# Optimization experiments

Hardware: AMD Instinct MI355X
Metric: run time of the kernel (lower is better)

Reference implementation:

```python
import jax, jax.numpy as jnp
import numpy as np

N_HEADS = 32
N_KV = 8
HEAD_DIM = 128
EPS = 1e-5

def _rope(t, fr, fi):
    # t: [b,s,h,hd] -> pairs [b,s,h,hd/2,2]; fr/fi: [s,hd/2]
    tp = t.astype(jnp.float32).reshape(*t.shape[:-1], HEAD_DIM // 2, 2)
    a, b = tp[..., 0], tp[..., 1]
    fr = fr[None, :, None, :]
    fi = fi[None, :, None, :]
    out = jnp.stack([a * fr - b * fi, a * fi + b * fr], axis=-1)
    return out.reshape(t.shape).astype(t.dtype)

def _rmsnorm(t):
    tf = t.astype(jnp.float32)
    return (tf * jax.lax.rsqrt(jnp.mean(tf * tf, axis=-1, keepdims=True) + EPS)).astype(t.dtype)

def setup_inputs() -> dict:
    key = jax.random.key(0)
    ks = jax.random.split(key, 5)
    b, s, dim = 1, 2048, 4096
    x = jax.random.normal(ks[0], (b, s, dim), dtype=jnp.float32) * 0.02
    wq = jax.random.normal(ks[1], (dim, dim), dtype=jnp.float32) * 0.02
    wk = jax.random.normal(ks[2], (N_KV * HEAD_DIM, dim), dtype=jnp.float32) * 0.02
    wv = jax.random.normal(ks[3], (N_KV * HEAD_DIM, dim), dtype=jnp.float32) * 0.02
    wo = jax.random.normal(ks[4], (dim, dim), dtype=jnp.float32) * 0.02
    # RoPE freqs, llama-style theta=10000
    inv = 1.0 / (10000.0 ** (np.arange(0, HEAD_DIM, 2, dtype=np.float32) / HEAD_DIM))
    ang = np.outer(np.arange(s, dtype=np.float32), inv)  # [s, hd/2]
    freqs_cis = jnp.asarray(np.stack([np.cos(ang), np.sin(ang)], axis=-1))  # [s, hd/2, 2]
    # causal additive mask
    mask = jnp.where(jnp.tril(jnp.ones((s, s), dtype=bool)), 0.0, -1e30).astype(jnp.float32)
    return {"x": x, "wq": wq, "wk": wk, "wv": wv, "wo": wo,
            "freqs_cis": freqs_cis, "mask": mask, "start_pos": 0}

def reference(x, wq, wk, wv, wo, freqs_cis, mask, start_pos):
    b, s, dim = x.shape
    n_rep = N_HEADS // N_KV
    xq = jnp.einsum('bsd,ed->bse', x, wq).reshape(b, s, N_HEADS, HEAD_DIM)
    xk = jnp.einsum('bsd,ed->bse', x, wk).reshape(b, s, N_KV, HEAD_DIM)
    xv = jnp.einsum('bsd,ed->bse', x, wv).reshape(b, s, N_KV, HEAD_DIM)
    fr, fi = freqs_cis[..., 0], freqs_cis[..., 1]
    xq = _rope(xq, fr, fi)
    xk = _rope(xk, fr, fi)
    xq = _rmsnorm(xq)
    xk = _rmsnorm(xk)
    # start_pos=0 prefill: KV cache write/read is identity on xk/xv
    q = xq.transpose(0, 2, 1, 3).reshape(b, N_KV, n_rep, s, HEAD_DIM)  # grouped query heads
    k = xk.transpose(0, 2, 1, 3)  # [b, n_kv, s, hd]
    v = xv.transpose(0, 2, 1, 3)
    scores = jnp.einsum('bkrsd,bktd->bkrst', q, k) / np.sqrt(HEAD_DIM)
    scores = scores + mask[None, None, None, :, :]
    probs = jax.nn.softmax(scores, axis=-1)
    o = jnp.einsum('bkrst,bktd->bkrsd', probs, v)
    o = o.reshape(b, N_HEADS, s, HEAD_DIM).transpose(0, 2, 1, 3).reshape(b, s, dim)
    return jnp.einsum('bse,de->bsd', o, wo)
```

## Files before the change

### kernel.cpp

```cpp
#include <hip/hip_runtime.h>
#include <hip/hip_bf16.h>
#include <cstdint>
#include <cstddef>

using u16 = unsigned short;
using u32 = unsigned int;
using u64 = unsigned long long;

typedef __attribute__((ext_vector_type(8))) __bf16 bf16x8;
typedef __attribute__((ext_vector_type(4))) float f32x4;
typedef __attribute__((ext_vector_type(2))) float f32x2;
typedef __attribute__((ext_vector_type(4))) u32 u32x4;

typedef const __attribute__((address_space(1))) void* gas_ptr;
typedef __attribute__((address_space(3))) void* las_ptr;

__device__ __forceinline__ void async_cp16(const void* g, void* l) {
  __builtin_amdgcn_global_load_lds((gas_ptr)g, (las_ptr)l, 16, 0, 0);
}

__device__ __forceinline__ float bf2f(u16 u) {
  u32 v = ((u32)u) << 16;
  return __builtin_bit_cast(float, v);
}
__device__ __forceinline__ u16 f2bf(float f) {
  u32 v = __builtin_bit_cast(u32, f);
  u32 r = (v + 0x7fffu + ((v >> 16) & 1u)) >> 16;
  return (u16)r;
}

__device__ __forceinline__ f32x4 mfma16(bf16x8 a, bf16x8 b, f32x4 c) {
  return __builtin_amdgcn_mfma_f32_16x16x32_bf16(a, b, c, 0, 0, 0);
}

__global__ __launch_bounds__(256) void cvt4(const float* __restrict__ x,
                                            const float* __restrict__ wq,
                                            const float* __restrict__ wk,
                                            const float* __restrict__ wv,
                                            u16* __restrict__ xb,
                                            u16* __restrict__ wqkv) {
  const int B0 = 1048576;
  const int B1 = B0 + 2097152;
  const int B2 = B1 + 524288;
  const int B3 = B2 + 524288;
  int i = blockIdx.x * blockDim.x + threadIdx.x;
  int stride = gridDim.x * blockDim.x;
  for (; i < B3; i += stride) {
    const float* src; u16* dst; int j;
    if (i < B0)      { src = x;  dst = xb;                           j = i; }
    else if (i < B1) { src = wq; dst = wqkv;                         j = i - B0; }
    else if (i < B2) { src = wk; dst = wqkv + (size_t)4096 * 4096;   j = i - B1; }
    else             { src = wv; dst = wqkv + (size_t)5120 * 4096;   j = i - B2; }
    const float4* p = (const float4*)(src + (size_t)j * 8);
    float4 a = p[0], b = p[1];
    union { u16 us[8]; u32x4 v; } o;
    o.us[0] = f2bf(a.x); o.us[1] = f2bf(a.y); o.us[2] = f2bf(a.z); o.us[3] = f2bf(a.w);
    o.us[4] = f2bf(b.x); o.us[5] = f2bf(b.y); o.us[6] = f2bf(b.z); o.us[7] = f2bf(b.w);
    *(u32x4*)(dst + (size_t)j * 8) = o.v;
  }
}

__global__ __launch_bounds__(512, 2) void gemm256(const u16* __restrict__ A,
                                                  const u16* __restrict__ B,
                                                  int M, int N, int K,
                                                  u16* __restrict__ qh,
                                                  u16* __restrict__ khh,
                                                  u16* __restrict__ vt,
                                                  const float* __restrict__ freqs) {
  __shared__ __align__(16) u16 As[2][16384];
  __shared__ __align__(16) u16 Bs[2][16384];
  const int tid = threadIdx.x;
  const int wave = tid >> 6, lane = tid & 63;
  const int quad = lane >> 4, c16 = lane & 15;
  const int wr = wave >> 2, wc = wave & 3;

  const int mb = M >> 8;
  const int nb = N >> 8;
  const int per_xcd_n = nb >> 3;
  const int xcd = blockIdx.x & 7, lid = blockIdx.x >> 3;
  const int m_t = lid % mb, n_local = lid / mb;
  const int m0 = m_t * 256, n0 = (xcd * per_xcd_n + n_local) * 256;

  const u16* Ab = A + (size_t)m0 * K;
  const u16* Bb = B + (size_t)n0 * K;

  f32x4 acc[8][4] = {};

  const int atg = wc * 64 + lane;
  const int bh = wc >> 1;
  const int btg = (((wr << 1) | (wc & 1)) << 6) + lane;

  auto stage_tile = [&](int k0, int b) __attribute__((always_inline)) {
#pragma unroll
    for (int j = 0; j < 4; ++j) {
      int idx = atg + 256 * j;
      int rl = idx >> 3;
      int row = wr * 128 + rl;
      int sg = (idx & 7) ^ (row & 7);
      async_cp16(Ab + (size_t)row * K + k0 + sg * 8, &As[b][wr * 8192 + idx * 8]);
    }
#pragma unroll
    for (int j = 0; j < 4; ++j) {
      int idx = btg + 256 * j;
      int rl = idx >> 3;
      int row = bh * 128 + rl;
      int sg = (idx & 7) ^ (row & 7);
      async_cp16(Bb + (size_t)row * K + k0 + sg * 8, &Bs[b][bh * 8192 + idx * 8]);
    }
  };

  bf16x8 bfr[4];
  auto phase = [&](int b, int ks, int mh, bool loadB) __attribute__((always_inline)) {
    bf16x8 af[4];
    if (loadB) {
#pragma unroll
      for (int nt = 0; nt < 4; ++nt) {
        int row = wc * 64 + nt * 16 + c16;
        bfr[nt] = *(const bf16x8*)(&Bs[b][row * 64 + (((ks * 4 + quad) ^ (row & 7)) * 8)]);
      }
    }
#pragma unroll
    for (int mt = 0; mt < 4; ++mt) {
      int row = wr * 128 + (mh * 4 + mt) * 16 + c16;
      af[mt] = *(const bf16x8*)(&As[b][row * 64 + (((ks * 4 + quad) ^ (row & 7)) * 8)]);
    }
    asm volatile("s_waitcnt lgkmcnt(0)" ::: "memory");
    __builtin_amdgcn_sched_barrier(0);
    __builtin_amdgcn_s_setprio(1);
#pragma unroll
    for (int mt = 0; mt < 4; ++mt)
#pragma unroll
      for (int nt = 0; nt < 4; ++nt)
        acc[mh * 4 + mt][nt] = mfma16(af[mt], bfr[nt], acc[mh * 4 + mt][nt]);
    __builtin_amdgcn_s_setprio(0);
    __builtin_amdgcn_s_barrier();
  };

  const int nk = K >> 6;
  stage_tile(0, 0);

#pragma unroll 1
  for (int t = 0; t < nk; ++t) {
    const int b = t & 1;
    const int k0 = t << 6;
    if (t + 1 < nk) {
      stage_tile(k0 + 64, b ^ 1);
      asm volatile("s_waitcnt vmcnt(8)" ::: "memory");
    } else {
      asm volatile("s_waitcnt vmcnt(0)" ::: "memory");
    }
    __builtin_amdgcn_s_barrier();
    phase(b, 0, 0, true);
    phase(b, 0, 1, false);
    phase(b, 1, 0, true);
    phase(b, 1, 1, false);
  }

  __syncthreads();
  float* sums = (float*)&As[0][0];
  if (n0 < 5120) {
    float ss_arr[8][4];
    const int dbase = (wc & 1) * 64;
#pragma unroll
    for (int mt = 0; mt < 8; ++mt) {
#pragma unroll
      for (int r = 0; r < 4; ++r) {
        int s = m0 + wr * 128 + mt * 16 + quad * 4 + r;
        const float* fb = freqs + (size_t)s * 128;
        float ssv = 0.0f;
#pragma unroll
        for (int nt = 0; nt < 4; ++nt) {
          int d = dbase + nt * 16 + c16;
          float v = acc[mt][nt][r];
          float p = __shfl_xor(v, 1, 64);
          f32x2 ff = *(const f32x2*)(fb + (d & ~1));
          float res = (c16 & 1) ? fmaf(v, ff.x, p * ff.y)
                                : fmaf(v, ff.x, -p * ff.y);
          acc[mt][nt][r] = res;
          ssv = fmaf(res, res, ssv);
        }
#pragma unroll
        for (int m = 1; m < 16; m <<= 1) ssv += __shfl_xor(ssv, m, 64);
        ss_arr[mt][r] = ssv;
      }
    }
    if (c16 == 0) {
#pragma unroll
      for (int mt = 0; mt < 8; ++mt)
#pragma unroll
        for (int r = 0; r < 4; ++r)
          sums[wc * 256 + wr * 128 + mt * 16 + quad * 4 + r] = ss_arr[mt][r];
    }
    __syncthreads();
    const int head_col = n0 + wc * 64;
    u16* outb = (head_col < 4096)
                    ? (qh + (size_t)(head_col >> 7) * M * 128)
                    : (khh + (size_t)((head_col - 4096) >> 7) * M * 128);
#pragma unroll
    for (int mt = 0; mt < 8; ++mt) {
#pragma unroll
      for (int r = 0; r < 4; ++r) {
        int rl = wr * 128 + mt * 16 + quad * 4 + r;
        float tot = ss_arr[mt][r] + sums[(wc ^ 1) * 256 + rl];
        float scl = rsqrtf(tot * (1.0f / 128.0f) + 1e-5f);
        int s = m0 + rl;
#pragma unroll
        for (int nt = 0; nt < 4; ++nt)
          outb[(size_t)s * 128 + dbase + nt * 16 + c16] = f2bf(acc[mt][nt][r] * scl);
      }
    }
  } else {
#pragma unroll
    for (int mt = 0; mt < 8; ++mt) {
#pragma unroll
      for (int nt = 0; nt < 4; ++nt) {
        int dv = (n0 - 5120) + wc * 64 + nt * 16 + c16;
        int s0 = m0 + wr * 128 + mt * 16 + quad * 4;
        union { u16 us[4]; u64 v; } pk;
#pragma unroll
        for (int r = 0; r < 4; ++r) pk.us[r] = f2bf(acc[mt][nt][r]);
        *(u64*)(vt + (size_t)dv * M + s0) = pk.v;
      }
    }
  }
}

__global__ __launch_bounds__(256, 3) void gemm_out(const u16* __restrict__ A,
                                                   const u16* __restrict__ B,
                                                   float* __restrict__ C,
                                                   int M, int N, int K) {
  __shared__ __align__(16) u16 As[128 * 64];
  __shared__ __align__(16) u16 Bs[128 * 64];
  const int tid = threadIdx.x;
  const int wave = tid >> 6, lane = tid & 63;
  const int quad = lane >> 4, c16 = lane & 15;

  const int mb = M >> 7, nb = N >> 7;
  const int per_xcd_n = nb >> 3;
  const int xcd = blockIdx.x & 7, lid = blockIdx.x >> 3;
  const int m_t = lid % mb, n_local = lid / mb;
  const int m0 = m_t * 128, n0 = (xcd * per_xcd_n + n_local) * 128;

  const int wm = (wave & 1) * 64, wn = (wave >> 1) * 64;

  f32x4 acc[4][4] = {};

  const u16* Ab = A + (size_t)m0 * K;
  const u16* Bb = B + (size_t)n0 * K;

  for (int k0 = 0; k0 < K; k0 += 64) {
    __syncthreads();
#pragma unroll
    for (int i = 0; i < 4; ++i) {
      int idx = tid + 256 * i;
      int row = idx >> 3, sg = (idx & 7) ^ (row & 7);
      async_cp16(Ab + (size_t)row * K + k0 + sg * 8, As + (size_t)idx * 8);
    }
#pragma unroll
    for (int i = 0; i < 4; ++i) {
      int idx = tid + 256 * i;
      int row = idx >> 3, sg = (idx & 7) ^ (row & 7);
      async_cp16(Bb + (size_t)row * K + k0 + sg * 8, Bs + (size_t)idx * 8);
    }
    asm volatile("s_waitcnt vmcnt(0)" ::: "memory");
    __syncthreads();

    bf16x8 af[4][2], bfr[4][2];
#pragma unroll
    for (int mt = 0; mt < 4; ++mt) {
      int row = wm + mt * 16 + c16;
#pragma unroll
      for (int c = 0; c < 2; ++c)
        af[mt][c] = *(const bf16x8*)(As + row * 64 + (((c * 4 + quad) ^ (row & 7)) * 8));
    }
#pragma unroll
    for (int nt = 0; nt < 4; ++nt) {
      int row = wn + nt * 16 + c16;
#pragma unroll
      for (int c = 0; c < 2; ++c)
        bfr[nt][c] = *(const bf16x8*)(Bs + row * 64 + (((c * 4 + quad) ^ (row & 7)) * 8));
    }
#pragma unroll
    for (int c = 0; c < 2; ++c)
#pragma unroll
      for (int mt = 0; mt < 4; ++mt)
#pragma unroll
        for (int nt = 0; nt < 4; ++nt)
          acc[mt][nt] = mfma16(af[mt][c], bfr[nt][c], acc[mt][nt]);
  }

#pragma unroll
  for (int mt = 0; mt < 4; ++mt) {
#pragma unroll
    for (int nt = 0; nt < 4; ++nt) {
#pragma unroll
      for (int r = 0; r < 4; ++r) {
        int gm = m0 + wm + mt * 16 + quad * 4 + r;
        int gn = n0 + wn + nt * 16 + c16;
        C[(size_t)gm * N + gn] = acc[mt][nt][r];
      }
    }
  }
}

#define SEQ 2048
__global__ __launch_bounds__(512, 2) void attn(const u16* __restrict__ Q,
                                               const u16* __restrict__ Kh,
                                               const u16* __restrict__ VT,
                                               u16* __restrict__ O,
                                               const float* __restrict__ wo,
                                               u16* __restrict__ wob) {
  __shared__ __align__(16) u16 Ks[2][64 * 128];
  __shared__ __align__(16) u16 Vs[2][128 * 64];
  __shared__ __align__(16) u16 Ps[8][32 * 64];
  const int tid = threadIdx.x;
  const int wave = tid >> 6, lane = tid & 63;
  const int quad = lane >> 4, c16 = lane & 15;
  const int bid = blockIdx.x;
  const int hk = bid & 7;
  const int rest = bid >> 3;
  const int hq = rest & 3;
  const int p = rest >> 2;
  const int h = hk * 4 + hq;

  const int wl = wave & 3, grp = wave >> 2;
  const int qt = grp ? p : (15 - p);
  const int q0w = qt * 128 + wl * 32;
  const int kend = (15 - p) * 128 + 128;

  const float sc = 0.12751743f;
  const float B = 16.5f;
  const u16* Kb = Kh + (size_t)hk * SEQ * 128;
  const u16* Vb = VT + (size_t)hk * 128 * SEQ;

  auto stage = [&](int t0, int b) __attribute__((always_inline)) {
#pragma unroll
    for (int i = 0; i < 2; ++i) {
      int idx = tid + 512 * i;
      int row = idx >> 4, sg = (idx & 15) ^ (row & 7);
      async_cp16(Kb + (size_t)(t0 + row) * 128 + sg * 8, &Ks[b][(size_t)idx * 8]);
    }
#pragma unroll
    for (int i = 0; i < 2; ++i) {
      int idx = tid + 512 * i;
      int row = idx >> 3, sg = (idx & 7) ^ (row & 7);
      async_cp16(Vb + (size_t)row * SEQ + t0 + sg * 8, &Vs[b][(size_t)idx * 8]);
    }
  };

  bf16x8 qfr[2][4];
  const u16* qbase = Q + (size_t)h * SEQ * 128;
#pragma unroll
  for (int g = 0; g < 2; ++g)
#pragma unroll
    for (int c = 0; c < 4; ++c)
      qfr[g][c] =
          *(const bf16x8*)(qbase + (size_t)(q0w + g * 16 + c16) * 128 + c * 32 + quad * 8);

  f32x4 o_acc[2][8] = {};
  float lsum[2][4] = {};

  stage(0, 0);

#pragma unroll 1
  for (int t0 = 0; t0 < kend; t0 += 64) {
    const int cur = (t0 >> 6) & 1;
    asm volatile("s_waitcnt vmcnt(0)" ::: "memory");
    __syncthreads();
    if (t0 + 64 < kend) stage(t0 + 64, cur ^ 1);

    if (t0 < q0w + 32) {
      f32x4 sa[2][4] = {};
      __builtin_amdgcn_s_setprio(1);
#pragma unroll
      for (int ct = 0; ct < 4; ++ct) {
        int t = ct * 16 + c16;
        int tbase = t * 128;
        int tsw = t & 7;
#pragma unroll
        for (int c = 0; c < 4; ++c) {
          bf16x8 kf = *(const bf16x8*)(&Ks[cur][tbase + (((c * 4 + quad) ^ tsw) * 8)]);
          sa[0][ct] = mfma16(qfr[0][c], kf, sa[0][ct]);
          sa[1][ct] = mfma16(qfr[1][c], kf, sa[1][ct]);
        }
      }
      __builtin_amdgcn_s_setprio(0);

      const bool diag = (t0 + 64 > q0w);
      auto soft = [&](bool masked) __attribute__((always_inline)) {
#pragma unroll
        for (int g = 0; g < 2; ++g) {
#pragma unroll
          for (int r = 0; r < 4; ++r) {
            int row = g * 16 + quad * 4 + r;
            int row_q = q0w + row;
            int rbase = row * 64;
            int rsw = row & 7;
#pragma unroll
            for (int ct = 0; ct < 4; ++ct) {
              float s = sa[g][ct][r];
              float arg = fmaf(s, sc, -B);
              if (masked) {
                int t_idx = t0 + ct * 16 + c16;
                arg = (t_idx <= row_q) ? arg : -1.0e30f;
              }
              float pe = exp2f(arg);
              lsum[g][r] += pe;
              u32 pb = (__builtin_bit_cast(u32, pe) + 0x8000u) >> 16;
              Ps[wave][rbase + (((ct * 2 + (c16 >> 3)) ^ rsw) * 8) + (c16 & 7)] = (u16)pb;
            }
          }
        }
      };
      if (diag) soft(true); else soft(false);
      asm volatile("s_waitcnt lgkmcnt(0)" ::: "memory");

      __builtin_amdgcn_s_setprio(1);
#pragma unroll
      for (int tc = 0; tc < 2; ++tc) {
        bf16x8 pf[2];
#pragma unroll
        for (int g = 0; g < 2; ++g) {
          int prow = g * 16 + c16;
          pf[g] = *(const bf16x8*)(&Ps[wave][prow * 64 + (((tc * 4 + quad) ^ (prow & 7)) * 8)]);
        }
#pragma unroll
        for (int nt = 0; nt < 8; ++nt) {
          int dl = nt * 16 + c16;
          bf16x8 vf = *(const bf16x8*)(&Vs[cur][dl * 64 + (((tc * 4 + quad) ^ (dl & 7)) * 8)]);
          o_acc[0][nt] = mfma16(pf[0], vf, o_acc[0][nt]);
          o_acc[1][nt] = mfma16(pf[1], vf, o_acc[1][nt]);
        }
      }
      __builtin_amdgcn_s_setprio(0);
    }
  }

#pragma unroll
  for (int g = 0; g < 2; ++g) {
#pragma unroll
    for (int r = 0; r < 4; ++r) {
      float l = lsum[g][r];
#pragma unroll
      for (int m = 1; m < 16; m <<= 1) l += __shfl_xor(l, m, 64);
      float inv = 1.0f / l;
      int s_idx = q0w + g * 16 + quad * 4 + r;
      u16* ob = O + (size_t)s_idx * 4096 + (size_t)h * 128;
#pragma unroll
      for (int nt = 0; nt < 8; ++nt) ob[nt * 16 + c16] = f2bf(o_acc[g][nt][r] * inv);
    }
  }

  {
    const int UNIT = 2341;
    const int N8 = 2097152;
    int su = 16 * p * (p - 1) + (bid & 31) * p;
    int i = su * UNIT + tid;
    int end = su * UNIT + p * UNIT;
    if (end > N8) end = N8;
    for (; i < end; i += 512) {
      const float4* src = (const float4*)(wo + (size_t)i * 8);
      float4 a = src[0], b = src[1];
      union { u16 us[8]; u32x4 v; } o;
      o.us[0] = f2bf(a.x); o.us[1] = f2bf(a.y); o.us[2] = f2bf(a.z); o.us[3] = f2bf(a.w);
      o.us[4] = f2bf(b.x); o.us[5] = f2bf(b.y); o.us[6] = f2bf(b.z); o.us[7] = f2bf(b.w);
      *(u32x4*)(wob + (size_t)i * 8) = o.v;
    }
  }
}

extern "C" void kernel_launch(void* const* d_in, const int* in_sizes, int n_in,
                              void* d_out, int out_size, void* d_ws, size_t ws_size,
                              hipStream_t stream) {
  const float* x  = (const float*)d_in[0];
  const float* wq = (const float*)d_in[1];
  const float* wk = (const float*)d_in[2];
  const float* wv = (const float*)d_in[3];
  const float* wo = (const float*)d_in[4];
  const float* fr = (const float*)d_in[5];
  float* out = (float*)d_out;

  const size_t S = 2048, D = 4096, KV = 1024, NQKV = D + 2 * KV;
  u16* p = (u16*)d_ws;
  u16* xb   = p; p += S * D;
  u16* wqkv = p; p += NQKV * D;
  u16* qh   = p; p += S * D;
  u16* khh  = p; p += S * KV;
  u16* vt   = p; p += KV * S;
  u16* ob   = p; p += S * D;
  u16* wob = wqkv;

  cvt4<<<dim3(2048), dim3(256), 0, stream>>>(x, wq, wk, wv, xb, wqkv);

  gemm256<<<dim3((S / 256) * (NQKV / 256)), dim3(512), 0, stream>>>(
      xb, wqkv, (int)S, (int)NQKV, (int)D, qh, khh, vt, fr);

  attn<<<dim3(256), dim3(512), 0, stream>>>(qh, khh, vt, ob, wo, wob);

  gemm_out<<<dim3((S / 128) * (D / 128)), dim3(256), 0, stream>>>(
      ob, wob, out, (int)S, (int)D, (int)D);
}
```

Baseline: 496.0 us.

## Restructure QKV GEMM main loop into 8-phase ping-pong pipeline with split-half staging

Rewrites the 256x256 GEMM main loop as an unrolled pair of K-tiles. Each iteration runs eight MFMA phases, with the global-to-LDS copies of A and B halves interleaved between the phases. It also loads all B fragments for a tile into registers at once, so the B fragments are no longer reloaded per phase. The aim is finer overlap of global loads with MFMA work. The cost is more barriers per iteration, more register use, and a hardcoded iteration count of 32, which assumes K=4096.

Result: faster. 468.3 us (-5.6%).

```diff
diff --git a/kernel.cpp b/kernel.cpp
--- a/kernel.cpp
+++ b/kernel.cpp
@@ -67,8 +67,8 @@
                                                   u16* __restrict__ khh,
                                                   u16* __restrict__ vt,
                                                   const float* __restrict__ freqs) {
-  __shared__ __align__(16) u16 As[2][16384];
-  __shared__ __align__(16) u16 Bs[2][16384];
+  __shared__ __align__(16) u16 As[2][2][8192];
+  __shared__ __align__(16) u16 Bs[2][2][8192];
   const int tid = threadIdx.x;
   const int wave = tid >> 6, lane = tid & 63;
   const int quad = lane >> 4, c16 = lane & 15;
@@ -85,79 +85,100 @@
   const u16* Bb = B + (size_t)n0 * K;
 
   f32x4 acc[8][4] = {};
-
-  const int atg = wc * 64 + lane;
-  const int bh = wc >> 1;
-  const int btg = (((wr << 1) | (wc & 1)) << 6) + lane;
-
-  auto stage_tile = [&](int k0, int b) __attribute__((always_inline)) {
-#pragma unroll
-    for (int j = 0; j < 4; ++j) {
-      int idx = atg + 256 * j;
+  bf16x8 breg[2][4];
+
+  auto stA = [&](int t, int h) __attribute__((always_inline)) {
+#pragma unroll
+    for (int j = 0; j < 2; ++j) {
+      int idx = tid + 512 * j;
       int rl = idx >> 3;
-      int row = wr * 128 + rl;
-      int sg = (idx & 7) ^ (row & 7);
-      async_cp16(Ab + (size_t)row * K + k0 + sg * 8, &As[b][wr * 8192 + idx * 8]);
-    }
-#pragma unroll
-    for (int j = 0; j < 4; ++j) {
-      int idx = btg + 256 * j;
+      int sg = (idx & 7) ^ (rl & 7);
+      async_cp16(Ab + (size_t)(h * 128 + rl) * K + (t << 6) + sg * 8,
+                 &As[t & 1][h][idx * 8]);
+    }
+  };
+  auto stB = [&](int t, int h) __attribute__((always_inline)) {
+#pragma unroll
+    for (int j = 0; j < 2; ++j) {
+      int idx = tid + 512 * j;
       int rl = idx >> 3;
-      int row = bh * 128 + rl;
-      int sg = (idx & 7) ^ (row & 7);
-      async_cp16(Bb + (size_t)row * K + k0 + sg * 8, &Bs[b][bh * 8192 + idx * 8]);
+      int sg = (idx & 7) ^ (rl & 7);
+      async_cp16(Bb + (size_t)(h * 128 + rl) * K + (t << 6) + sg * 8,
+                 &Bs[t & 1][h][idx * 8]);
     }
   };
-
-  bf16x8 bfr[4];
-  auto phase = [&](int b, int ks, int mh, bool loadB) __attribute__((always_inline)) {
-    bf16x8 af[4];
-    if (loadB) {
+  auto ldA = [&](bf16x8* a, int par, int mh, int ks) __attribute__((always_inline)) {
+#pragma unroll
+    for (int mt = 0; mt < 4; ++mt) {
+      int rl = mh * 64 + mt * 16 + c16;
+      a[mt] = *(const bf16x8*)(&As[par][wr][rl * 64 + (((ks * 4 + quad) ^ (rl & 7)) * 8)]);
+    }
+  };
+  auto ldB = [&](int par) __attribute__((always_inline)) {
+#pragma unroll
+    for (int ks = 0; ks < 2; ++ks)
 #pragma unroll
       for (int nt = 0; nt < 4; ++nt) {
-        int row = wc * 64 + nt * 16 + c16;
-        bfr[nt] = *(const bf16x8*)(&Bs[b][row * 64 + (((ks * 4 + quad) ^ (row & 7)) * 8)]);
-      }
-    }
-#pragma unroll
-    for (int mt = 0; mt < 4; ++mt) {
-      int row = wr * 128 + (mh * 4 + mt) * 16 + c16;
-      af[mt] = *(const bf16x8*)(&As[b][row * 64 + (((ks * 4 + quad) ^ (row & 7)) * 8)]);
-    }
-    asm volatile("s_waitcnt lgkmcnt(0)" ::: "memory");
-    __builtin_amdgcn_sched_barrier(0);
+        int rl = (wc & 1) * 64 + nt * 16 + c16;
+        breg[ks][nt] =
+            *(const bf16x8*)(&Bs[par][wc >> 1][rl * 64 + (((ks * 4 + quad) ^ (rl & 7)) * 8)]);
+      }
+  };
+  auto mm = [&](bf16x8* a, int mh, int ks) __attribute__((always_inline)) {
     __builtin_amdgcn_s_setprio(1);
 #pragma unroll
     for (int mt = 0; mt < 4; ++mt)
 #pragma unroll
       for (int nt = 0; nt < 4; ++nt)
-        acc[mh * 4 + mt][nt] = mfma16(af[mt], bfr[nt], acc[mh * 4 + mt][nt]);
+        acc[mh * 4 + mt][nt] = mfma16(a[mt], breg[ks][nt], acc[mh * 4 + mt][nt]);
     __builtin_amdgcn_s_setprio(0);
-    __builtin_amdgcn_s_barrier();
   };
 
-  const int nk = K >> 6;
-  stage_tile(0, 0);
+#define BARX() asm volatile("s_barrier" ::: "memory")
+#define LGKM0()                                        \
+  asm volatile("s_waitcnt lgkmcnt(0)" ::: "memory");   \
+  __builtin_amdgcn_sched_barrier(0)
+
+  stA(0, 0); stA(0, 1); stB(0, 0); stB(0, 1);
+  stA(1, 0); stA(1, 1); stB(1, 0); stB(1, 1);
+  asm volatile("s_waitcnt vmcnt(0)" ::: "memory");
+  BARX();
 
 #pragma unroll 1
-  for (int t = 0; t < nk; ++t) {
-    const int b = t & 1;
-    const int k0 = t << 6;
-    if (t + 1 < nk) {
-      stage_tile(k0 + 64, b ^ 1);
-      asm volatile("s_waitcnt vmcnt(8)" ::: "memory");
-    } else {
-      asm volatile("s_waitcnt vmcnt(0)" ::: "memory");
-    }
-    __builtin_amdgcn_s_barrier();
-    phase(b, 0, 0, true);
-    phase(b, 0, 1, false);
-    phase(b, 1, 0, true);
-    phase(b, 1, 1, false);
-  }
+  for (int i = 0; i < 32; ++i) {
+    bf16x8 a[4];
+    ldB(0); ldA(a, 0, 0, 0);
+    if (i >= 1) { stA(2 * i + 1, 0); stA(2 * i + 1, 1); }
+    BARX(); LGKM0(); mm(a, 0, 0); BARX();
+    ldA(a, 0, 1, 0);
+    if (2 * i + 2 < 64) stB(2 * i + 2, 0);
+    BARX(); LGKM0(); mm(a, 1, 0); BARX();
+    ldA(a, 0, 0, 1);
+    if (2 * i + 2 < 64) stB(2 * i + 2, 1);
+    BARX(); LGKM0(); mm(a, 0, 1); BARX();
+    ldA(a, 0, 1, 1);
+    if (i < 31) asm volatile("s_waitcnt vmcnt(4)" ::: "memory");
+    else        asm volatile("s_waitcnt vmcnt(0)" ::: "memory");
+    BARX(); LGKM0(); mm(a, 1, 1); BARX();
+    ldB(1); ldA(a, 1, 0, 0);
+    if (2 * i + 2 < 64) stA(2 * i + 2, 0);
+    BARX(); LGKM0(); mm(a, 0, 0); BARX();
+    ldA(a, 1, 1, 0);
+    if (2 * i + 2 < 64) stA(2 * i + 2, 1);
+    BARX(); LGKM0(); mm(a, 1, 0); BARX();
+    ldA(a, 1, 0, 1);
+    if (2 * i + 3 < 64) stB(2 * i + 3, 0);
+    BARX(); LGKM0(); mm(a, 0, 1); BARX();
+    ldA(a, 1, 1, 1);
+    if (2 * i + 3 < 64) stB(2 * i + 3, 1);
+    if (i < 31) asm volatile("s_waitcnt vmcnt(4)" ::: "memory");
+    BARX(); LGKM0(); mm(a, 1, 1); BARX();
+  }
+#undef BARX
+#undef LGKM0
 
   __syncthreads();
-  float* sums = (float*)&As[0][0];
+  float* sums = (float*)&As[0][0][0];
   if (n0 < 5120) {
     float ss_arr[8][4];
     const int dbase = (wc & 1) * 64;
```
